# Performance work log

Hardware: AMD Instinct MI355X
Metric: run time of the kernel (lower is better)

Reference implementation:

```python
import math
import jax, jax.numpy as jnp
import numpy as np

LEVELS = 4          # wavelet_levels
PRUNE = 0.05        # wavelet_packet_prune_ratio
EPS = 1e-6
SQRT2 = math.sqrt(2.0)


def _haar_split(c):
    n = c.shape[-1]
    if n % 2 != 0:
        c = jnp.concatenate([c, jnp.zeros(c.shape[:-1] + (1,), c.dtype)], axis=-1)
    even, odd = c[..., 0::2], c[..., 1::2]
    return (even + odd) / SQRT2, (even - odd) / SQRT2, n


def _haar_merge(low, high, orig):
    even = (low + high) / SQRT2
    odd = (low - high) / SQRT2
    out = jnp.stack([even, odd], axis=-1).reshape(*low.shape[:-1], low.shape[-1] * 2)
    return out[..., :orig]


def _coherence(c, gpu):
    unit = c / jnp.maximum(jnp.abs(c), EPS)
    return jnp.clip(jnp.abs(jnp.mean(unit * jnp.conj(gpu), axis=-1, keepdims=True)), 0.0, 1.0)


def _cost(c, gpu):
    # gauge-aware packet cost: Shannon entropy of energy distribution + (1 - coherence)
    if c.shape[-1] <= 1:
        return jnp.float32(0.0)
    e = jnp.square(jnp.abs(c))
    p = jnp.maximum(e / jnp.maximum(e.sum(-1, keepdims=True), EPS), EPS)
    ent = -(p * jnp.log(p)).sum(-1)
    coh = _coherence(c, gpu)[..., 0]
    return jax.lax.stop_gradient(jnp.mean(ent + (1.0 - coh)))


def _band_center(path):
    if not path:
        return 0.0
    idx = 0
    for b in path:
        idx = (idx << 1) | b
    return (idx + 0.5) / (2 ** len(path))


def _leaf_gain(c, path, depth, gpu, Wp, bp, Wo, bo, lfg, sigma, hfg, cutoff):
    mag = jnp.maximum(jnp.abs(c), EPS)
    phase = jnp.arctan2(c.imag, c.real) / math.pi
    nle = jnp.broadcast_to(
        jnp.log(jnp.maximum(jnp.mean(jnp.square(jnp.abs(c)), -1, keepdims=True), EPS)), mag.shape)
    dn = jnp.full(mag.shape, depth / max(1, LEVELS), mag.dtype)
    bcv = _band_center(path)
    bc = jnp.full(mag.shape, bcv, mag.dtype)
    coh = jnp.broadcast_to(_coherence(c, gpu), mag.shape)
    pos = jnp.broadcast_to(jnp.linspace(0.0, 1.0, c.shape[-1], dtype=mag.dtype), mag.shape)
    feats = jnp.stack([jnp.log(mag), phase, nle, dn, bc, coh, pos], axis=-1)  # [..., n, 7]
    gd = jax.nn.silu(feats @ Wp.T + bp) @ Wo.T + bo                            # [..., n, 2]
    dm = 0.25 * jnp.tanh(gd[..., 0])
    dp = 0.5 * math.pi * jnp.tanh(gd[..., 1])
    lbb = 1.0 + lfg * jnp.exp(-(bcv * bcv) / jnp.square(sigma))
    hbd = hfg + (1.0 - hfg) * jax.nn.sigmoid((cutoff - bcv) / sigma)
    gm = lbb * hbd * (1.0 + lfg * coh) * (hfg + (1.0 - hfg) * coh) * jnp.exp(dm)
    return jax.lax.complex(gm * jnp.cos(dp), gm * jnp.sin(dp))  # torch.polar


def _filter_leaf(c, path, depth, total_e, gpu, params):
    Wp, bp, Wo, bo, lfg, sigma, hfg, cutoff = params
    node_e = jax.lax.stop_gradient(jnp.square(jnp.abs(c)).sum())
    filtered = c * _leaf_gain(c, path, depth, gpu, Wp, bp, Wo, bo, lfg, sigma, hfg, cutoff)
    coh_v = jax.lax.stop_gradient(jnp.mean(_coherence(c, gpu)))
    # spectral subtraction
    fm = jnp.abs(filtered)
    nf = jnp.median(fm, axis=-1, keepdims=True)
    damping = hfg + (1.0 - hfg) * jax.nn.sigmoid((cutoff - _band_center(path)) / sigma)
    den = jax.nn.relu(fm - (1.0 - damping) * nf)
    filtered = den * (filtered / jnp.maximum(fm, EPS))
    # prune low-energy / low-coherence leaves
    prune = jnp.logical_or(node_e / total_e < PRUNE, coh_v < PRUNE)
    return jnp.where(prune, filtered * jnp.square(hfg), filtered)


def _apply_node(c, depth, path, total_e, gpu, params):
    cost = _cost(c, gpu)
    leaf = _filter_leaf(c, path, depth, total_e, gpu, params)
    if depth >= LEVELS or c.shape[-1] <= 1:
        return leaf, cost
    low, high, orig = _haar_split(c)
    lr, lc = _apply_node(low, depth + 1, path + (0,), total_e, gpu, params)
    hr, hc = _apply_node(high, depth + 1, path + (1,), total_e, gpu, params)
    merged = _haar_merge(lr, hr, orig)
    child_cost = lc + hc
    # best-basis selection (wavelet_packet_best_basis=True)
    out = jnp.where(child_cost < cost, merged, leaf)
    return out, jnp.minimum(child_cost, cost)


def setup_inputs() -> dict:
    key = jax.random.key(0)
    ks = jax.random.split(key, 3)
    B, R, N = 8, 64, 8192
    x = jax.random.normal(ks[0], (B, R, N), jnp.float32)
    Wp = jax.random.normal(ks[1], (12, 7), jnp.float32) * math.sqrt(2.0 / 19.0)  # xavier-ish
    bp = jnp.zeros((12,), jnp.float32)
    Wo = jax.random.normal(ks[2], (2, 12), jnp.float32) * 0.1
    bo = jnp.zeros((2,), jnp.float32)
    return {"x": x, "Wp": Wp, "bp": bp, "Wo": Wo, "bo": bo,
            "lfg": jnp.float32(0.5), "sigma": jnp.float32(0.3),
            "hfg": jnp.float32(0.7), "cutoff": jnp.float32(0.25)}


def reference(x, Wp, bp, Wo, bo, lfg, sigma, hfg, cutoff):
    n = x.shape[-1]
    spec = jnp.fft.fft(x)  # complex64 [B, R, N]
    # _fft_filter spectral gating
    r2 = jnp.square(jnp.fft.fftfreq(n).astype(x.dtype))
    lfb = 1.0 + lfg * jnp.exp(-r2 / jnp.square(sigma))
    radius = jnp.sqrt(r2 + 1e-12)
    gate = jax.nn.sigmoid((cutoff - radius) / jnp.maximum(sigma, 0.05))
    spec = spec * (lfb * (hfg + (1.0 - hfg) * gate))
    # global phase unit
    unit = spec / jnp.maximum(jnp.abs(spec), EPS)
    g = jnp.mean(unit, axis=-1, keepdims=True)
    gpu = g / jnp.maximum(jnp.abs(g), EPS)
    total_e = jax.lax.stop_gradient(jnp.square(jnp.abs(spec)).sum())
    params = (Wp, bp, Wo, bo, lfg, sigma, hfg, cutoff)
    out, _ = _apply_node(spec, 0, (), total_e, gpu, params)
    return jnp.fft.ifft(out).real
```

## Files before the change

kernel.cpp:

```cpp
#include <hip/hip_runtime.h>
#include <math.h>

#define NN      8192
#define LOGN    13
#define ROWS    512
#define NT      512
#define NNODES  31
#define EPSF    1e-6f
#define PRUNEF  0.05f
#define SQRT1_2F 0.70710678118654752f
#define PIF      3.14159265358979323f
#define INV_PIF  0.31830988618379067f
#define HALF_PIF 1.57079632679489662f

typedef unsigned int uint;

__device__ __forceinline__ float fast_rcp(float x){ return __builtin_amdgcn_rcpf(x); }
__device__ __forceinline__ float fast_rsq(float x){ return __builtin_amdgcn_rsqf(x); }

__device__ __forceinline__ float tanh_fast(float x){
    float e = __expf(2.f * x);
    return 1.f - 2.f * fast_rcp(e + 1.f);
}
__device__ __forceinline__ float silu_pade(float h){
    float y = fminf(3.f, fmaxf(-3.f, 0.5f * h));
    float y2 = y * y;
    float num = y * fmaf(y2, 10.f, 105.f);
    float den = fmaf(y2, 45.f, fmaf(y2 * y2, 1.f, 105.f));
    return 0.5f * h * (1.f + num * fast_rcp(den));
}
__device__ __forceinline__ float exp_small(float z){
    return fmaf(z, fmaf(z, fmaf(z, fmaf(z, 0.041666667f, 0.16666667f), 0.5f), 1.f), 1.f);
}

__device__ __forceinline__ float fast_atan2f(float y, float x) {
    float ay = fabsf(y), ax = fabsf(x);
    float mx = fmaxf(ax, ay), mn = fminf(ax, ay);
    float a = (mx > 0.f) ? (mn * fast_rcp(mx)) : 0.f;
    bool big = a > 0.4142135679f;
    float t = big ? ((a - 1.f) * fast_rcp(a + 1.f)) : a;
    float z2 = t * t;
    float p = fmaf(8.05374449538e-2f, z2, -1.38776856032e-1f);
    p = fmaf(p, z2, 1.99777106478e-1f);
    p = fmaf(p, z2, -3.33329491539e-1f);
    float r = fmaf(p * z2, t, t);
    if (big) r += 0.78539816339744831f;
    if (ay > ax) r = 1.57079632679489662f - r;
    if (x < 0.f) r = 3.14159265358979323f - r;
    return copysignf(r, y);
}

__device__ __forceinline__ float2 cmul(float2 a, float2 b){
    return make_float2(a.x*b.x - a.y*b.y, a.x*b.y + a.y*b.x);
}
__device__ __forceinline__ float2 cadd(float2 a, float2 b){ return make_float2(a.x+b.x, a.y+b.y); }
__device__ __forceinline__ float2 csub(float2 a, float2 b){ return make_float2(a.x-b.x, a.y-b.y); }

__device__ __forceinline__ void wave_red8(float* a) {
    #pragma unroll
    for (int m = 32; m >= 1; m >>= 1) {
        #pragma unroll
        for (int q = 0; q < 8; ++q) a[q] += __shfl_xor(a[q], m);
    }
}

__global__ __launch_bounds__(NT, 4) void k_pre(
    const float* __restrict__ x, float2* __restrict__ Lv,
    float* __restrict__ Se, float* __restrict__ Coh, float* __restrict__ Ent,
    const float* lfg_p, const float* sig_p, const float* hfg_p, const float* cut_p)
{
    __shared__ float2 sh[NN];
    __shared__ float4 wred[8];
    __shared__ float nacc[16][4];
    int row = blockIdx.x, tid = threadIdx.x;
    float lfg = *lfg_p, sigma = *sig_p, hfg = *hfg_p, cutoff = *cut_p;

    const float* xr = x + ((size_t)row << LOGN);
    #pragma unroll
    for (int t = 0; t < 16; ++t) {
        int i = tid + (t << 9);
        sh[i] = make_float2(xr[i], 0.f);
    }
    __syncthreads();

    for (int sp = 0; sp < 6; ++sp) {
        int lg = 11 - 2 * sp;
        int Hh = 1 << lg;
        float angf = -PIF / (float)(2 * Hh);
        #pragma unroll 4
        for (int c = 0; c < 4; ++c) {
            int q = tid + (c << 9);
            int j = q & (Hh - 1);
            int p = ((q >> lg) << (lg + 2)) | j;
            float2 a = sh[p], b = sh[p + Hh], cc = sh[p + 2 * Hh], d = sh[p + 3 * Hh];
            float ang = angf * (float)j;
            float s = __sinf(ang), co = __cosf(ang);
            float2 t1 = make_float2(co, s);
            float2 t2 = make_float2(co * co - s * s, 2.f * co * s);
            float2 a1 = cadd(a, cc);
            float2 c1 = cmul(csub(a, cc), t1);
            float2 b1 = cadd(b, d);
            float2 u  = cmul(csub(b, d), t1);
            float2 d1 = make_float2(u.y, -u.x);
            sh[p]          = cadd(a1, b1);
            sh[p + Hh]     = cmul(csub(a1, b1), t2);
            sh[p + 2 * Hh] = cadd(c1, d1);
            sh[p + 3 * Hh] = cmul(csub(c1, d1), t2);
        }
        __syncthreads();
    }
    #pragma unroll 8
    for (int c = 0; c < 8; ++c) {
        int p = (tid + (c << 9)) << 1;
        float2 a = sh[p], b = sh[p + 1];
        sh[p] = cadd(a, b);
        sh[p + 1] = csub(a, b);
    }
    __syncthreads();

    float inv_gs = 1.f / fmaxf(sigma, 0.05f);
    float is2 = 1.f / (sigma * sigma);
    float se = 0.f, slg = 0.f, sux = 0.f, suy = 0.f;
    #pragma unroll
    for (int t = 0; t < 16; ++t) {
        int p = tid + (t << 9);
        int k = (int)(__brev((uint)p) >> 19);
        float fk = (k < NN / 2) ? (float)k : (float)(k - NN);
        float f = fk * (1.0f / (float)NN);
        float r2 = f * f;
        float lfb = 1.f + lfg * __expf(-r2 * is2);
        float radius = sqrtf(r2 + 1e-12f);
        float gate = fast_rcp(1.f + __expf(-(cutoff - radius) * inv_gs));
        float mult = lfb * (hfg + (1.f - hfg) * gate);
        float2 c = sh[p];
        c.x *= mult; c.y *= mult;
        sh[p] = c;
        float e = fmaf(c.x, c.x, c.y * c.y);
        se += e;
        slg += e * __logf(fmaxf(e, 1e-30f));
        float inv = fminf(fast_rsq(e), 1e6f);
        sux += c.x * inv; suy += c.y * inv;
    }
    #pragma unroll
    for (int m = 32; m >= 1; m >>= 1) {
        se += __shfl_xor(se, m); slg += __shfl_xor(slg, m);
        sux += __shfl_xor(sux, m); suy += __shfl_xor(suy, m);
    }
    if ((tid & 63) == 0) wred[tid >> 6] = make_float4(se, slg, sux, suy);
    __syncthreads();
    if (tid == 0) {
        float4 r = wred[0];
        #pragma unroll
        for (int w = 1; w < 8; ++w) {
            r.x += wred[w].x; r.y += wred[w].y; r.z += wred[w].z; r.w += wred[w].w;
        }
        float gx = r.z / (float)NN, gy = r.w / (float)NN;
        float ga = sqrtf(gx * gx + gy * gy);
        float denom = fmaxf(r.x, EPSF);
        Se[row]  = r.x;
        Ent[row] = __logf(denom) - r.y / denom;
        Coh[row] = fminf(ga, 1.f);
    }

    for (int dp = 0; dp < 4; ++dp) {
        int shn = 12 - dp;
        int h = 1 << shn;
        int fim1 = (1 << (3 - dp)) - 1;
        if (tid < 64) ((float*)nacc)[tid] = 0.f;
        __syncthreads();
        float acc[8] = {0,0,0,0,0,0,0,0};
        #pragma unroll
        for (int t = 0; t < 8; ++t) {
            int q = tid + (t << 9);
            int p = ((q & ~(h - 1)) << 1) | (q & (h - 1));
            float2 a = sh[p], b = sh[p + h];
            float2 lo = make_float2((a.x + b.x) * SQRT1_2F, (a.y + b.y) * SQRT1_2F);
            float2 hi = make_float2((a.x - b.x) * SQRT1_2F, (a.y - b.y) * SQRT1_2F);
            sh[p] = lo; sh[p + h] = hi;
            float e1 = fmaf(lo.x, lo.x, lo.y * lo.y);
            acc[0] += e1; acc[1] += e1 * __logf(fmaxf(e1, 1e-30f));
            float i1 = fminf(fast_rsq(e1), 1e6f);
            acc[2] += lo.x * i1; acc[3] += lo.y * i1;
            float e2 = fmaf(hi.x, hi.x, hi.y * hi.y);
            acc[4] += e2; acc[5] += e2 * __logf(fmaxf(e2, 1e-30f));
            float i2 = fminf(fast_rsq(e2), 1e6f);
            acc[6] += hi.x * i2; acc[7] += hi.y * i2;
            if (((t + 1) & fim1) == 0) {
                wave_red8(acc);
                if ((tid & 63) == 0) {
                    int ca = (q >> shn) << 1;
                    atomicAdd(&nacc[ca][0], acc[0]);   atomicAdd(&nacc[ca][1], acc[1]);
                    atomicAdd(&nacc[ca][2], acc[2]);   atomicAdd(&nacc[ca][3], acc[3]);
                    atomicAdd(&nacc[ca+1][0], acc[4]); atomicAdd(&nacc[ca+1][1], acc[5]);
                    atomicAdd(&nacc[ca+1][2], acc[6]); atomicAdd(&nacc[ca+1][3], acc[7]);
                }
                #pragma unroll
                for (int qq = 0; qq < 8; ++qq) acc[qq] = 0.f;
            }
        }
        __syncthreads();
        int cn = 2 << dp;
        if (tid < cn) {
            float E = nacc[tid][0], SL = nacc[tid][1], ZX = nacc[tid][2], ZY = nacc[tid][3];
            float denom = fmaxf(E, EPSF);
            float ent = __logf(denom) - SL / denom;
            float invn = 1.f / (float)(1 << shn);
            float zx = ZX * invn, zy = ZY * invn;
            float ch = fminf(sqrtf(zx * zx + zy * zy), 1.f);
            int g = cn - 1 + tid;
            Se[g * ROWS + row] = E; Coh[g * ROWS + row] = ch; Ent[g * ROWS + row] = ent;
        }
        __syncthreads();
    }

    float4* lrow = (float4*)(Lv + ((size_t)row << LOGN));
    const float4* s4 = (const float4*)sh;
    #pragma unroll
    for (int t = 0; t < 8; ++t) { int k = tid + (t << 9); lrow[k] = s4[k]; }
}

__device__ __forceinline__ uint key_at(const float2* sh, int p) {
    float2 v = sh[p];
    return __float_as_uint(fmaf(v.x, v.x, v.y * v.y));
}

__device__ __forceinline__ uint2 hist_locate1024(
    const uint* hist, int tid, uint r, uint* wsum, uint* selres)
{
    uint l0 = hist[2 * tid], l1 = hist[2 * tid + 1];
    uint s = l0 + l1;
    uint sc = s;
    #pragma unroll
    for (int o = 1; o < 64; o <<= 1) {
        uint v = __shfl_up(sc, o);
        if ((tid & 63) >= o) sc += v;
    }
    int wid = tid >> 6;
    if ((tid & 63) == 63) wsum[wid] = sc;
    __syncthreads();
    uint wb = 0;
    #pragma unroll
    for (int w = 0; w < 8; ++w) if (w < wid) wb += wsum[w];
    uint c0 = wb + sc - s;
    if (r >= c0 && r < c0 + l0) { selres[0] = 2u * tid;      selres[1] = c0; }
    c0 += l0;
    if (r >= c0 && r < c0 + l1) { selres[0] = 2u * tid + 1u; selres[1] = c0; }
    __syncthreads();
    uint2 res = make_uint2(selres[0], selres[1]);
    __syncthreads();
    return res;
}

__device__ float median_node(
    const float2* sh, int eb, int ept, int nd, int tid,
    uint* hist, uint* wsum, uint* selres)
{
    uint r1 = (uint)(nd / 2 - 1), r2 = (uint)(nd / 2);
    for (int k = tid; k < 1024; k += NT) hist[k] = 0u;
    __syncthreads();
    for (int c = 0; c < ept; ++c)
        atomicAdd(&hist[key_at(sh, eb + tid + (c << 9)) >> 21], 1u);
    __syncthreads();
    uint2 A1 = hist_locate1024(hist, tid, r1, wsum, selres);
    uint2 A2 = hist_locate1024(hist, tid, r2, wsum, selres);
    uint va, vb;
    if (A1.x != A2.x) {
        if (tid == 0) { selres[0] = 0u; selres[1] = 0xFFFFFFFFu; }
        __syncthreads();
        for (int c = 0; c < ept; ++c) {
            uint k = key_at(sh, eb + tid + (c << 9));
            uint b = k >> 21;
            if (b == A1.x) atomicMax(&selres[0], k);
            if (b == A2.x) atomicMin(&selres[1], k);
        }
        __syncthreads();
        va = selres[0]; vb = selres[1];
        __syncthreads();
    } else {
        uint p1 = A1.x;
        for (int k = tid; k < 1024; k += NT) hist[k] = 0u;
        __syncthreads();
        for (int c = 0; c < ept; ++c) {
            uint k = key_at(sh, eb + tid + (c << 9));
            if ((k >> 21) == p1) atomicAdd(&hist[(k >> 11) & 1023u], 1u);
        }
        __syncthreads();
        uint2 B1 = hist_locate1024(hist, tid, r1 - A1.y, wsum, selres);
        uint2 B2 = hist_locate1024(hist, tid, r2 - A1.y, wsum, selres);
        if (B1.x != B2.x) {
            uint pA = (p1 << 10) | B1.x, pB = (p1 << 10) | B2.x;
            if (tid == 0) { selres[0] = 0u; selres[1] = 0xFFFFFFFFu; }
            __syncthreads();
            for (int c = 0; c < ept; ++c) {
                uint k = key_at(sh, eb + tid + (c << 9));
                uint b = k >> 11;
                if (b == pA) atomicMax(&selres[0], k);
                if (b == pB) atomicMin(&selres[1], k);
            }
            __syncthreads();
            va = selres[0]; vb = selres[1];
            __syncthreads();
        } else {
            uint pfx = (p1 << 10) | B1.x;
            for (int k = tid; k < 1024; k += NT) hist[k] = 0u;
            __syncthreads();
            for (int c = 0; c < ept; ++c) {
                uint k = key_at(sh, eb + tid + (c << 9));
                if ((k >> 11) == pfx) atomicAdd(&hist[(k >> 1) & 1023u], 1u);
            }
            __syncthreads();
            uint2 C1 = hist_locate1024(hist, tid, r1 - A1.y - B1.y, wsum, selres);
            uint2 C2 = hist_locate1024(hist, tid, r2 - A1.y - B1.y, wsum, selres);
            va = ((pfx << 10) | C1.x) << 1;
            vb = ((pfx << 10) | C2.x) << 1;
        }
    }
    return 0.5f * (sqrtf(__uint_as_float(va)) + sqrtf(__uint_as_float(vb)));
}

__device__ __forceinline__ void dev_decide(
    const float* __restrict__ Se, const float* __restrict__ Coh, const float* __restrict__ Ent,
    int tid, float* dtmp, int* fF, int* fP)
{
    float* dcost = dtmp; float* dne = dtmp + NNODES; float* dcm = dtmp + 2 * NNODES;
    int wid = tid >> 6, lane = tid & 63;
    for (int gn = wid; gn < NNODES; gn += 8) {
        float a = 0.f, b = 0.f, cc = 0.f;
        #pragma unroll
        for (int rr = 0; rr < ROWS / 64; ++rr) {
            int r = lane + (rr << 6);
            float ch = Coh[gn * ROWS + r];
            a += Ent[gn * ROWS + r] + 1.f - ch;
            b += Se[gn * ROWS + r];
            cc += ch;
        }
        #pragma unroll
        for (int m = 32; m >= 1; m >>= 1) {
            a += __shfl_xor(a, m); b += __shfl_xor(b, m); cc += __shfl_xor(cc, m);
        }
        if (lane == 0) { dcost[gn] = a / (float)ROWS; dne[gn] = b; dcm[gn] = cc / (float)ROWS; }
    }
    __syncthreads();
    if (tid == 0) {
        float mc[NNODES]; int sel[NNODES]; int act[NNODES];
        for (int gn = NNODES - 1; gn >= 0; --gn) {
            if (gn >= 15) { mc[gn] = dcost[gn]; sel[gn] = 0; }
            else {
                float chc = mc[2 * gn + 1] + mc[2 * gn + 2];
                sel[gn] = (chc < dcost[gn]) ? 1 : 0;
                mc[gn] = fminf(chc, dcost[gn]);
            }
        }
        float total_e = dne[0];
        act[0] = 1;
        for (int gn = 1; gn < NNODES; ++gn) {
            int p = (gn - 1) >> 1;
            act[gn] = act[p] && sel[p];
        }
        for (int gn = 0; gn < NNODES; ++gn) {
            int isleaf = (gn >= 15);
            fF[gn] = (act[gn] && (isleaf || !sel[gn])) ? 1 : 0;
            fP[gn] = ((dne[gn] / total_e < PRUNEF) || (dcm[gn] < PRUNEF)) ? 1 : 0;
        }
    }
    __syncthreads();
}

__device__ void filter_node(
    float2* sh, int d, int n, int tid,
    const float* wsh, const float* sSe, const float* sCoh, const int* fP,
    uint* hist, uint* wsum, uint* selres,
    float lfg, float sigma, float hfg, float cutoff)
{
    int lognd = LOGN - d;
    int nd = 1 << lognd;
    int ept = nd >> 9;
    int g = (1 << d) - 1 + n;
    int eb = n << lognd;
    float bcv = (d == 0) ? 0.f : ((float)n + 0.5f) / (float)(1 << d);
    float coh = sCoh[g], sev = sSe[g];
    float nle = __logf(fmaxf(sev / (float)nd, EPSF));
    float dnv = (float)d * 0.25f;
    float lbb = 1.f + lfg * __expf(-(bcv * bcv) / (sigma * sigma));
    float hbd = hfg + (1.f - hfg) * fast_rcp(1.f + __expf(-(cutoff - bcv) / sigma));
    float gbase = lbb * hbd * (1.f + lfg * coh) * (hfg + (1.f - hfg) * coh);
    float invnm1 = 1.f / (float)(nd - 1);
    float w0r[12], w1r[12], w6r[12], wo0r[12], wo1r[12], hb[12];
    #pragma unroll
    for (int j = 0; j < 12; ++j) {
        w0r[j] = wsh[j*7+0]; w1r[j] = wsh[j*7+1]; w6r[j] = wsh[j*7+6];
        wo0r[j] = wsh[96+j]; wo1r[j] = wsh[108+j];
        hb[j] = wsh[84+j] + nle*wsh[j*7+2] + dnv*wsh[j*7+3] + bcv*wsh[j*7+4] + coh*wsh[j*7+5];
    }
    float bo0 = wsh[120], bo1 = wsh[121];

    for (int c = 0; c < ept; ++c) {
        int o = tid + (c << 9);
        int p = eb + o;
        float2 cv = sh[p];
        float m2 = fmaf(cv.x, cv.x, cv.y * cv.y);
        float f0 = 0.5f * __logf(fmaxf(m2, 1e-12f));
        float f1 = fast_atan2f(cv.y, cv.x) * INV_PIF;
        int itrue = (int)(__brev((uint)o) >> (19 + d));
        float f6 = (float)itrue * invnm1;
        float acc0 = bo0, acc1 = bo1;
        #pragma unroll
        for (int j = 0; j < 12; ++j) {
            float h = fmaf(f0, w0r[j], fmaf(f1, w1r[j], fmaf(f6, w6r[j], hb[j])));
            float s = silu_pade(h);
            acc0 = fmaf(s, wo0r[j], acc0);
            acc1 = fmaf(s, wo1r[j], acc1);
        }
        float gm = gbase * exp_small(0.25f * tanh_fast(acc0));
        float dph = HALF_PIF * tanh_fast(acc1);
        float spv, cpv;
        __sincosf(dph, &spv, &cpv);
        float fr = gm * (cv.x * cpv - cv.y * spv);
        float fi = gm * (cv.x * spv + cv.y * cpv);
        sh[p] = make_float2(fr, fi);
    }
    __syncthreads();

    float nf = median_node(sh, eb, ept, nd, tid, hist, wsum, selres);
    float thr = (1.f - hbd) * nf;
    float pf = fP[g] ? (hfg * hfg) : 1.f;

    for (int c = 0; c < ept; ++c) {
        int p = eb + tid + (c << 9);
        float2 v = sh[p];
        float fm = sqrtf(fmaf(v.x, v.x, v.y * v.y));
        float den = fmaxf(fm - thr, 0.f);
        float s = den * fast_rcp(fmaxf(fm, EPSF)) * pf;
        sh[p] = make_float2(v.x * s, v.y * s);
    }
    __syncthreads();
}

__global__ __launch_bounds__(NT, 4) void k_rest(
    const float2* __restrict__ Lv,
    const float* __restrict__ Se, const float* __restrict__ Coh, const float* __restrict__ Ent,
    float* __restrict__ out,
    const float* __restrict__ Wp, const float* __restrict__ bp,
    const float* __restrict__ Wo, const float* __restrict__ bo,
    const float* lfg_p, const float* sig_p, const float* hfg_p, const float* cut_p)
{
    __shared__ float2 sh[NN];
    __shared__ __align__(16) uint hist[1024];
    __shared__ float wsh[122];
    __shared__ float sSe[NNODES], sCoh[NNODES];
    __shared__ int fF[NNODES], fP[NNODES];
    __shared__ float dtmp[3 * NNODES];
    __shared__ uint wsum[8];
    __shared__ uint selres[2];

    int row = blockIdx.x, tid = threadIdx.x;
    float lfg = *lfg_p, sigma = *sig_p, hfg = *hfg_p, cutoff = *cut_p;

    const float4* lrow = (const float4*)(Lv + ((size_t)row << LOGN));
    float4* s4 = (float4*)sh;
    #pragma unroll
    for (int t = 0; t < 8; ++t) { int k = tid + (t << 9); s4[k] = lrow[k]; }

    if (tid < 122) wsh[tid] = (tid < 84) ? Wp[tid] : (tid < 96) ? bp[tid - 84]
                            : (tid < 120) ? Wo[tid - 96] : bo[tid - 120];
    if (tid < NNODES) { sSe[tid] = Se[tid * ROWS + row]; sCoh[tid] = Coh[tid * ROWS + row]; }

    dev_decide(Se, Coh, Ent, tid, dtmp, fF, fP);

    for (int n = 0; n < 16; ++n)
        if (fF[15 + n])
            filter_node(sh, 4, n, tid, wsh, sSe, sCoh, fP, hist, wsum, selres, lfg, sigma, hfg, cutoff);

    for (int d = 3; d >= 0; --d) {
        int h = 1 << (12 - d);
        #pragma unroll
        for (int t = 0; t < 8; ++t) {
            int q = tid + (t << 9);
            int p = ((q & ~(h - 1)) << 1) | (q & (h - 1));
            float2 lo = sh[p], hi = sh[p + h];
            sh[p]     = make_float2((lo.x + hi.x) * SQRT1_2F, (lo.y + hi.y) * SQRT1_2F);
            sh[p + h] = make_float2((lo.x - hi.x) * SQRT1_2F, (lo.y - hi.y) * SQRT1_2F);
        }
        __syncthreads();
        for (int n = 0; n < (1 << d); ++n)
            if (fF[(1 << d) - 1 + n])
                filter_node(sh, d, n, tid, wsh, sSe, sCoh, fP, hist, wsum, selres, lfg, sigma, hfg, cutoff);
    }

    for (int sp = 0; sp < 6; ++sp) {
        int h = 1 << (2 * sp);
        float angf = PIF / (float)(2 * h);
        #pragma unroll 4
        for (int c = 0; c < 4; ++c) {
            int q = tid + (c << 9);
            int jj = q & (h - 1);
            int p0 = ((q >> (2 * sp)) << (2 * sp + 2)) | jj;
            float ang = angf * (float)jj;
            float s2 = __sinf(ang), c2 = __cosf(ang);
            float2 t2 = make_float2(c2, s2);
            float2 t1 = make_float2(c2 * c2 - s2 * s2, 2.f * c2 * s2);
            float2 a = sh[p0], b = sh[p0 + h], cc = sh[p0 + 2 * h], d = sh[p0 + 3 * h];
            float2 tb = cmul(t1, b);
            float2 ap = cadd(a, tb), bp2 = csub(a, tb);
            float2 td = cmul(t1, d);
            float2 cp = cadd(cc, td), dp2 = csub(cc, td);
            float2 tc = cmul(t2, cp);
            float2 u  = cmul(t2, dp2);
            float2 iB = make_float2(-u.y, u.x);
            sh[p0]         = cadd(ap, tc);
            sh[p0 + h]     = cadd(bp2, iB);
            sh[p0 + 2 * h] = csub(ap, tc);
            sh[p0 + 3 * h] = csub(bp2, iB);
        }
        __syncthreads();
    }
    {
        float angf = PIF / 4096.f;
        #pragma unroll 8
        for (int c = 0; c < 8; ++c) {
            int p = tid + (c << 9);
            float ang = angf * (float)p;
            float s = __sinf(ang), co = __cosf(ang);
            float2 a = sh[p], b = sh[p + 4096];
            float2 tb = cmul(make_float2(co, s), b);
            sh[p] = cadd(a, tb);
            sh[p + 4096] = csub(a, tb);
        }
        __syncthreads();
    }
    float* orow = out + ((size_t)row << LOGN);
    #pragma unroll
    for (int t = 0; t < 16; ++t) {
        int i = tid + (t << 9);
        orow[i] = sh[i].x * (1.0f / (float)NN);
    }
}

extern "C" void kernel_launch(void* const* d_in, const int* in_sizes, int n_in,
                              void* d_out, int out_size, void* d_ws, size_t ws_size,
                              hipStream_t stream) {
    const float* x   = (const float*)d_in[0];
    const float* Wp  = (const float*)d_in[1];
    const float* bp  = (const float*)d_in[2];
    const float* Wo  = (const float*)d_in[3];
    const float* bo  = (const float*)d_in[4];
    const float* lfg = (const float*)d_in[5];
    const float* sig = (const float*)d_in[6];
    const float* hfg = (const float*)d_in[7];
    const float* cut = (const float*)d_in[8];
    float* out = (float*)d_out;

    size_t S = (size_t)ROWS * NN * sizeof(float2);
    char* ws = (char*)d_ws;
    float2* Lv = (float2*)ws;
    float*  Se  = (float*)(ws + S);
    float*  Coh = Se  + (size_t)NNODES * ROWS;
    float*  Ent = Coh + (size_t)NNODES * ROWS;
    size_t need = (size_t)((char*)(Ent + (size_t)NNODES * ROWS) - ws);
    if (ws_size < need) return;

    dim3 b(NT);
    k_pre <<<dim3(ROWS), b, 0, stream>>>(x, Lv, Se, Coh, Ent, lfg, sig, hfg, cut);
    k_rest<<<dim3(ROWS), b, 0, stream>>>(Lv, Se, Coh, Ent, out, Wp, bp, Wo, bo, lfg, sig, hfg, cut);
}
```

Before: 138.2 us.

## Store intermediate spectrum in fp16, hoist tree decision, keep coefficients in registers

The intermediate spectrum passed between kernels is now stored as packed half2 instead of float2, halving that global traffic. The per-block tree-decision reduction, which every block repeated over all rows, moves into a single-block kernel whose flags are read back by each block. The Haar merge levels and per-node filtering now keep coefficients in registers, with templated depths, and only stage through shared memory for the filter and median steps. The fp16 storage loses precision in the spectrum, which can move median thresholds and the final output, and the register-resident arrays raise register pressure.

New measurement: 156.6 us. +13.4%, slower.

```diff
diff --git a/kernel.cpp b/kernel.cpp
--- a/kernel.cpp
+++ b/kernel.cpp
@@ -1,4 +1,5 @@
 #include <hip/hip_runtime.h>
+#include <hip/hip_fp16.h>
 #include <math.h>
 
 #define NN      8192
@@ -56,6 +57,15 @@
 __device__ __forceinline__ float2 cadd(float2 a, float2 b){ return make_float2(a.x+b.x, a.y+b.y); }
 __device__ __forceinline__ float2 csub(float2 a, float2 b){ return make_float2(a.x-b.x, a.y-b.y); }
 
+__device__ __forceinline__ uint pack_h2(float2 v){
+    __half2 h = __floats2half2_rn(v.x, v.y);
+    return __builtin_bit_cast(uint, h);
+}
+__device__ __forceinline__ float2 unpack_h2(uint u){
+    __half2 h = __builtin_bit_cast(__half2, u);
+    return make_float2(__low2float(h), __high2float(h));
+}
+
 __device__ __forceinline__ void wave_red8(float* a) {
     #pragma unroll
     for (int m = 32; m >= 1; m >>= 1) {
@@ -65,7 +75,7 @@
 }
 
 __global__ __launch_bounds__(NT, 4) void k_pre(
-    const float* __restrict__ x, float2* __restrict__ Lv,
+    const float* __restrict__ x, uint* __restrict__ Lv16,
     float* __restrict__ Se, float* __restrict__ Coh, float* __restrict__ Ent,
     const float* lfg_p, const float* sig_p, const float* hfg_p, const float* cut_p)
 {
@@ -213,10 +223,64 @@
         __syncthreads();
     }
 
-    float4* lrow = (float4*)(Lv + ((size_t)row << LOGN));
-    const float4* s4 = (const float4*)sh;
-    #pragma unroll
-    for (int t = 0; t < 8; ++t) { int k = tid + (t << 9); lrow[k] = s4[k]; }
+    uint* lrow = Lv16 + ((size_t)row << LOGN);
+    #pragma unroll
+    for (int t = 0; t < 16; ++t) {
+        int k = tid + (t << 9);
+        lrow[k] = pack_h2(sh[k]);
+    }
+}
+
+__global__ __launch_bounds__(NT) void k_decide(
+    const float* __restrict__ Se, const float* __restrict__ Coh, const float* __restrict__ Ent,
+    int* __restrict__ fFg, int* __restrict__ fPg)
+{
+    __shared__ float dtmp[3 * NNODES];
+    __shared__ int fF[NNODES], fP[NNODES];
+    int tid = threadIdx.x;
+    float* dcost = dtmp; float* dne = dtmp + NNODES; float* dcm = dtmp + 2 * NNODES;
+    int wid = tid >> 6, lane = tid & 63;
+    for (int gn = wid; gn < NNODES; gn += 8) {
+        float a = 0.f, b = 0.f, cc = 0.f;
+        #pragma unroll
+        for (int rr = 0; rr < ROWS / 64; ++rr) {
+            int r = lane + (rr << 6);
+            float ch = Coh[gn * ROWS + r];
+            a += Ent[gn * ROWS + r] + 1.f - ch;
+            b += Se[gn * ROWS + r];
+            cc += ch;
+        }
+        #pragma unroll
+        for (int m = 32; m >= 1; m >>= 1) {
+            a += __shfl_xor(a, m); b += __shfl_xor(b, m); cc += __shfl_xor(cc, m);
+        }
+        if (lane == 0) { dcost[gn] = a / (float)ROWS; dne[gn] = b; dcm[gn] = cc / (float)ROWS; }
+    }
+    __syncthreads();
+    if (tid == 0) {
+        float mc[NNODES]; int sel[NNODES]; int act[NNODES];
+        for (int gn = NNODES - 1; gn >= 0; --gn) {
+            if (gn >= 15) { mc[gn] = dcost[gn]; sel[gn] = 0; }
+            else {
+                float chc = mc[2 * gn + 1] + mc[2 * gn + 2];
+                sel[gn] = (chc < dcost[gn]) ? 1 : 0;
+                mc[gn] = fminf(chc, dcost[gn]);
+            }
+        }
+        float total_e = dne[0];
+        act[0] = 1;
+        for (int gn = 1; gn < NNODES; ++gn) {
+            int p = (gn - 1) >> 1;
+            act[gn] = act[p] && sel[p];
+        }
+        for (int gn = 0; gn < NNODES; ++gn) {
+            int isleaf = (gn >= 15);
+            fF[gn] = (act[gn] && (isleaf || !sel[gn])) ? 1 : 0;
+            fP[gn] = ((dne[gn] / total_e < PRUNEF) || (dcm[gn] < PRUNEF)) ? 1 : 0;
+        }
+    }
+    __syncthreads();
+    if (tid < NNODES) { fFg[tid] = fF[tid]; fPg[tid] = fP[tid]; }
 }
 
 __device__ __forceinline__ uint key_at(const float2* sh, int p) {
@@ -252,14 +316,14 @@
 }
 
 __device__ float median_node(
-    const float2* sh, int eb, int ept, int nd, int tid,
+    const float2* sh, int ept, int nd, int tid,
     uint* hist, uint* wsum, uint* selres)
 {
     uint r1 = (uint)(nd / 2 - 1), r2 = (uint)(nd / 2);
     for (int k = tid; k < 1024; k += NT) hist[k] = 0u;
     __syncthreads();
     for (int c = 0; c < ept; ++c)
-        atomicAdd(&hist[key_at(sh, eb + tid + (c << 9)) >> 21], 1u);
+        atomicAdd(&hist[key_at(sh, tid + (c << 9)) >> 21], 1u);
     __syncthreads();
     uint2 A1 = hist_locate1024(hist, tid, r1, wsum, selres);
     uint2 A2 = hist_locate1024(hist, tid, r2, wsum, selres);
@@ -268,7 +332,7 @@
         if (tid == 0) { selres[0] = 0u; selres[1] = 0xFFFFFFFFu; }
         __syncthreads();
         for (int c = 0; c < ept; ++c) {
-            uint k = key_at(sh, eb + tid + (c << 9));
+            uint k = key_at(sh, tid + (c << 9));
             uint b = k >> 21;
             if (b == A1.x) atomicMax(&selres[0], k);
             if (b == A2.x) atomicMin(&selres[1], k);
@@ -281,7 +345,7 @@
         for (int k = tid; k < 1024; k += NT) hist[k] = 0u;
         __syncthreads();
         for (int c = 0; c < ept; ++c) {
-            uint k = key_at(sh, eb + tid + (c << 9));
+            uint k = key_at(sh, tid + (c << 9));
             if ((k >> 21) == p1) atomicAdd(&hist[(k >> 11) & 1023u], 1u);
         }
         __syncthreads();
@@ -292,7 +356,7 @@
             if (tid == 0) { selres[0] = 0u; selres[1] = 0xFFFFFFFFu; }
             __syncthreads();
             for (int c = 0; c < ept; ++c) {
-                uint k = key_at(sh, eb + tid + (c << 9));
+                uint k = key_at(sh, tid + (c << 9));
                 uint b = k >> 11;
                 if (b == pA) atomicMax(&selres[0], k);
                 if (b == pB) atomicMin(&selres[1], k);
@@ -305,7 +369,7 @@
             for (int k = tid; k < 1024; k += NT) hist[k] = 0u;
             __syncthreads();
             for (int c = 0; c < ept; ++c) {
-                uint k = key_at(sh, eb + tid + (c << 9));
+                uint k = key_at(sh, tid + (c << 9));
                 if ((k >> 11) == pfx) atomicAdd(&hist[(k >> 1) & 1023u], 1u);
             }
             __syncthreads();
@@ -318,73 +382,33 @@
     return 0.5f * (sqrtf(__uint_as_float(va)) + sqrtf(__uint_as_float(vb)));
 }
 
-__device__ __forceinline__ void dev_decide(
-    const float* __restrict__ Se, const float* __restrict__ Coh, const float* __restrict__ Ent,
-    int tid, float* dtmp, int* fF, int* fP)
-{
-    float* dcost = dtmp; float* dne = dtmp + NNODES; float* dcm = dtmp + 2 * NNODES;
-    int wid = tid >> 6, lane = tid & 63;
-    for (int gn = wid; gn < NNODES; gn += 8) {
-        float a = 0.f, b = 0.f, cc = 0.f;
-        #pragma unroll
-        for (int rr = 0; rr < ROWS / 64; ++rr) {
-            int r = lane + (rr << 6);
-            float ch = Coh[gn * ROWS + r];
-            a += Ent[gn * ROWS + r] + 1.f - ch;
-            b += Se[gn * ROWS + r];
-            cc += ch;
-        }
-        #pragma unroll
-        for (int m = 32; m >= 1; m >>= 1) {
-            a += __shfl_xor(a, m); b += __shfl_xor(b, m); cc += __shfl_xor(cc, m);
-        }
-        if (lane == 0) { dcost[gn] = a / (float)ROWS; dne[gn] = b; dcm[gn] = cc / (float)ROWS; }
-    }
-    __syncthreads();
-    if (tid == 0) {
-        float mc[NNODES]; int sel[NNODES]; int act[NNODES];
-        for (int gn = NNODES - 1; gn >= 0; --gn) {
-            if (gn >= 15) { mc[gn] = dcost[gn]; sel[gn] = 0; }
-            else {
-                float chc = mc[2 * gn + 1] + mc[2 * gn + 2];
-                sel[gn] = (chc < dcost[gn]) ? 1 : 0;
-                mc[gn] = fminf(chc, dcost[gn]);
-            }
-        }
-        float total_e = dne[0];
-        act[0] = 1;
-        for (int gn = 1; gn < NNODES; ++gn) {
-            int p = (gn - 1) >> 1;
-            act[gn] = act[p] && sel[p];
-        }
-        for (int gn = 0; gn < NNODES; ++gn) {
-            int isleaf = (gn >= 15);
-            fF[gn] = (act[gn] && (isleaf || !sel[gn])) ? 1 : 0;
-            fP[gn] = ((dne[gn] / total_e < PRUNEF) || (dcm[gn] < PRUNEF)) ? 1 : 0;
-        }
-    }
-    __syncthreads();
-}
-
-__device__ void filter_node(
-    float2* sh, int d, int n, int tid,
+template<int D>
+__device__ void filter_node_reg(
+    float2 (&v)[16], int n, int tid, float2* sh,
     const float* wsh, const float* sSe, const float* sCoh, const int* fP,
     uint* hist, uint* wsum, uint* selres,
     float lfg, float sigma, float hfg, float cutoff)
 {
-    int lognd = LOGN - d;
-    int nd = 1 << lognd;
-    int ept = nd >> 9;
-    int g = (1 << d) - 1 + n;
-    int eb = n << lognd;
-    float bcv = (d == 0) ? 0.f : ((float)n + 0.5f) / (float)(1 << d);
+    constexpr int CNT = 16 >> D;
+    constexpr int ND  = NN >> D;
+    constexpr int EPT = ND >> 9;
+    int g = (1 << D) - 1 + n;
+
+    #pragma unroll
+    for (int t = 0; t < 16; ++t) {
+        int k = t - n * CNT;
+        if ((unsigned)k < (unsigned)CNT) sh[tid + (k << 9)] = v[t];
+    }
+    __syncthreads();
+
+    float bcv = (D == 0) ? 0.f : ((float)n + 0.5f) / (float)(1 << D);
     float coh = sCoh[g], sev = sSe[g];
-    float nle = __logf(fmaxf(sev / (float)nd, EPSF));
-    float dnv = (float)d * 0.25f;
+    float nle = __logf(fmaxf(sev / (float)ND, EPSF));
+    float dnv = (float)D * 0.25f;
     float lbb = 1.f + lfg * __expf(-(bcv * bcv) / (sigma * sigma));
     float hbd = hfg + (1.f - hfg) * fast_rcp(1.f + __expf(-(cutoff - bcv) / sigma));
     float gbase = lbb * hbd * (1.f + lfg * coh) * (hfg + (1.f - hfg) * coh);
-    float invnm1 = 1.f / (float)(nd - 1);
+    float invnm1 = 1.f / (float)(ND - 1);
     float w0r[12], w1r[12], w6r[12], wo0r[12], wo1r[12], hb[12];
     #pragma unroll
     for (int j = 0; j < 12; ++j) {
@@ -394,14 +418,14 @@
     }
     float bo0 = wsh[120], bo1 = wsh[121];
 
-    for (int c = 0; c < ept; ++c) {
+    #pragma unroll
+    for (int c = 0; c < EPT; ++c) {
         int o = tid + (c << 9);
-        int p = eb + o;
-        float2 cv = sh[p];
+        float2 cv = sh[o];
         float m2 = fmaf(cv.x, cv.x, cv.y * cv.y);
         float f0 = 0.5f * __logf(fmaxf(m2, 1e-12f));
         float f1 = fast_atan2f(cv.y, cv.x) * INV_PIF;
-        int itrue = (int)(__brev((uint)o) >> (19 + d));
+        int itrue = (int)(__brev((uint)o) >> (19 + D));
         float f6 = (float)itrue * invnm1;
         float acc0 = bo0, acc1 = bo1;
         #pragma unroll
@@ -417,28 +441,49 @@
         __sincosf(dph, &spv, &cpv);
         float fr = gm * (cv.x * cpv - cv.y * spv);
         float fi = gm * (cv.x * spv + cv.y * cpv);
-        sh[p] = make_float2(fr, fi);
-    }
-    __syncthreads();
-
-    float nf = median_node(sh, eb, ept, nd, tid, hist, wsum, selres);
+        sh[o] = make_float2(fr, fi);
+    }
+    __syncthreads();
+
+    float nf = median_node(sh, EPT, ND, tid, hist, wsum, selres);
     float thr = (1.f - hbd) * nf;
     float pf = fP[g] ? (hfg * hfg) : 1.f;
 
-    for (int c = 0; c < ept; ++c) {
-        int p = eb + tid + (c << 9);
-        float2 v = sh[p];
-        float fm = sqrtf(fmaf(v.x, v.x, v.y * v.y));
+    #pragma unroll
+    for (int c = 0; c < EPT; ++c) {
+        int o = tid + (c << 9);
+        float2 w = sh[o];
+        float fm = sqrtf(fmaf(w.x, w.x, w.y * w.y));
         float den = fmaxf(fm - thr, 0.f);
         float s = den * fast_rcp(fmaxf(fm, EPSF)) * pf;
-        sh[p] = make_float2(v.x * s, v.y * s);
-    }
-    __syncthreads();
+        sh[o] = make_float2(w.x * s, w.y * s);
+    }
+    __syncthreads();
+
+    #pragma unroll
+    for (int t = 0; t < 16; ++t) {
+        int k = t - n * CNT;
+        if ((unsigned)k < (unsigned)CNT) v[t] = sh[tid + (k << 9)];
+    }
+    __syncthreads();
+}
+
+template<int DT>
+__device__ __forceinline__ void merge_reg(float2 (&v)[16]){
+    #pragma unroll
+    for (int t = 0; t < 16; ++t) {
+        if ((t & DT) == 0) {
+            float2 lo = v[t], hi = v[t + DT];
+            v[t]      = make_float2((lo.x + hi.x) * SQRT1_2F, (lo.y + hi.y) * SQRT1_2F);
+            v[t + DT] = make_float2((lo.x - hi.x) * SQRT1_2F, (lo.y - hi.y) * SQRT1_2F);
+        }
+    }
 }
 
 __global__ __launch_bounds__(NT, 4) void k_rest(
-    const float2* __restrict__ Lv,
-    const float* __restrict__ Se, const float* __restrict__ Coh, const float* __restrict__ Ent,
+    const uint* __restrict__ Lv16,
+    const float* __restrict__ Se, const float* __restrict__ Coh,
+    const int* __restrict__ fFg, const int* __restrict__ fPg,
     float* __restrict__ out,
     const float* __restrict__ Wp, const float* __restrict__ bp,
     const float* __restrict__ Wo, const float* __restrict__ bo,
@@ -449,43 +494,54 @@
     __shared__ float wsh[122];
     __shared__ float sSe[NNODES], sCoh[NNODES];
     __shared__ int fF[NNODES], fP[NNODES];
-    __shared__ float dtmp[3 * NNODES];
     __shared__ uint wsum[8];
     __shared__ uint selres[2];
 
     int row = blockIdx.x, tid = threadIdx.x;
     float lfg = *lfg_p, sigma = *sig_p, hfg = *hfg_p, cutoff = *cut_p;
 
-    const float4* lrow = (const float4*)(Lv + ((size_t)row << LOGN));
-    float4* s4 = (float4*)sh;
-    #pragma unroll
-    for (int t = 0; t < 8; ++t) { int k = tid + (t << 9); s4[k] = lrow[k]; }
+    const uint* lr = Lv16 + ((size_t)row << LOGN);
+    uint raw[16];
+    #pragma unroll
+    for (int t = 0; t < 16; ++t) raw[t] = lr[tid + (t << 9)];
 
     if (tid < 122) wsh[tid] = (tid < 84) ? Wp[tid] : (tid < 96) ? bp[tid - 84]
                             : (tid < 120) ? Wo[tid - 96] : bo[tid - 120];
-    if (tid < NNODES) { sSe[tid] = Se[tid * ROWS + row]; sCoh[tid] = Coh[tid * ROWS + row]; }
-
-    dev_decide(Se, Coh, Ent, tid, dtmp, fF, fP);
+    if (tid < NNODES) {
+        sSe[tid] = Se[tid * ROWS + row];
+        sCoh[tid] = Coh[tid * ROWS + row];
+        fF[tid] = fFg[tid];
+        fP[tid] = fPg[tid];
+    }
+    __syncthreads();
+
+    float2 v[16];
+    #pragma unroll
+    for (int t = 0; t < 16; ++t) v[t] = unpack_h2(raw[t]);
 
     for (int n = 0; n < 16; ++n)
         if (fF[15 + n])
-            filter_node(sh, 4, n, tid, wsh, sSe, sCoh, fP, hist, wsum, selres, lfg, sigma, hfg, cutoff);
-
-    for (int d = 3; d >= 0; --d) {
-        int h = 1 << (12 - d);
-        #pragma unroll
-        for (int t = 0; t < 8; ++t) {
-            int q = tid + (t << 9);
-            int p = ((q & ~(h - 1)) << 1) | (q & (h - 1));
-            float2 lo = sh[p], hi = sh[p + h];
-            sh[p]     = make_float2((lo.x + hi.x) * SQRT1_2F, (lo.y + hi.y) * SQRT1_2F);
-            sh[p + h] = make_float2((lo.x - hi.x) * SQRT1_2F, (lo.y - hi.y) * SQRT1_2F);
-        }
-        __syncthreads();
-        for (int n = 0; n < (1 << d); ++n)
-            if (fF[(1 << d) - 1 + n])
-                filter_node(sh, d, n, tid, wsh, sSe, sCoh, fP, hist, wsum, selres, lfg, sigma, hfg, cutoff);
-    }
+            filter_node_reg<4>(v, n, tid, sh, wsh, sSe, sCoh, fP, hist, wsum, selres, lfg, sigma, hfg, cutoff);
+
+    merge_reg<1>(v);
+    for (int n = 0; n < 8; ++n)
+        if (fF[7 + n])
+            filter_node_reg<3>(v, n, tid, sh, wsh, sSe, sCoh, fP, hist, wsum, selres, lfg, sigma, hfg, cutoff);
+    merge_reg<2>(v);
+    for (int n = 0; n < 4; ++n)
+        if (fF[3 + n])
+            filter_node_reg<2>(v, n, tid, sh, wsh, sSe, sCoh, fP, hist, wsum, selres, lfg, sigma, hfg, cutoff);
+    merge_reg<4>(v);
+    for (int n = 0; n < 2; ++n)
+        if (fF[1 + n])
+            filter_node_reg<1>(v, n, tid, sh, wsh, sSe, sCoh, fP, hist, wsum, selres, lfg, sigma, hfg, cutoff);
+    merge_reg<8>(v);
+    if (fF[0])
+        filter_node_reg<0>(v, 0, tid, sh, wsh, sSe, sCoh, fP, hist, wsum, selres, lfg, sigma, hfg, cutoff);
+
+    #pragma unroll
+    for (int t = 0; t < 16; ++t) sh[tid + (t << 9)] = v[t];
+    __syncthreads();
 
     for (int sp = 0; sp < 6; ++sp) {
         int h = 1 << (2 * sp);
@@ -550,16 +606,19 @@
     const float* cut = (const float*)d_in[8];
     float* out = (float*)d_out;
 
-    size_t S = (size_t)ROWS * NN * sizeof(float2);
+    size_t LVB = (size_t)ROWS * NN * sizeof(uint);
     char* ws = (char*)d_ws;
-    float2* Lv = (float2*)ws;
-    float*  Se  = (float*)(ws + S);
-    float*  Coh = Se  + (size_t)NNODES * ROWS;
-    float*  Ent = Coh + (size_t)NNODES * ROWS;
-    size_t need = (size_t)((char*)(Ent + (size_t)NNODES * ROWS) - ws);
+    uint*   Lv16 = (uint*)ws;
+    float*  Se   = (float*)(ws + LVB);
+    float*  Coh  = Se  + (size_t)NNODES * ROWS;
+    float*  Ent  = Coh + (size_t)NNODES * ROWS;
+    int*    fFg  = (int*)(Ent + (size_t)NNODES * ROWS);
+    int*    fPg  = fFg + NNODES;
+    size_t need = (size_t)((char*)(fPg + NNODES) - ws);
     if (ws_size < need) return;
 
     dim3 b(NT);
-    k_pre <<<dim3(ROWS), b, 0, stream>>>(x, Lv, Se, Coh, Ent, lfg, sig, hfg, cut);
-    k_rest<<<dim3(ROWS), b, 0, stream>>>(Lv, Se, Coh, Ent, out, Wp, bp, Wo, bo, lfg, sig, hfg, cut);
-}
+    k_pre   <<<dim3(ROWS), b, 0, stream>>>(x, Lv16, Se, Coh, Ent, lfg, sig, hfg, cut);
+    k_decide<<<dim3(1),    b, 0, stream>>>(Se, Coh, Ent, fFg, fPg);
+    k_rest  <<<dim3(ROWS), b, 0, stream>>>(Lv16, Se, Coh, fFg, fPg, out, Wp, bp, Wo, bo, lfg, sig, hfg, cut);
+}
```
